# Kernel tuning notes

Hardware: AMD Instinct MI355X
Metric: run time of the kernel (lower is better)

## Reference

```python
import jax, jax.numpy as jnp
import numpy as np

DIM = 1024

def setup_inputs() -> dict:
    key = jax.random.key(0)
    k1, k2, k3, k4, k5 = jax.random.split(key, 5)
    x = jax.random.normal(k1, (8, 2048, DIM), dtype=jnp.float32)
    # nn.Linear-style params: W is [out, in], b is [out]
    s = 1.0 / np.sqrt(DIM)
    W1 = jax.random.uniform(k2, (DIM, DIM), jnp.float32, -s, s)
    b1 = jax.random.uniform(k3, (DIM,), jnp.float32, -s, s)
    W2 = jax.random.uniform(k4, (DIM, DIM), jnp.float32, -s, s)
    b2 = jax.random.uniform(k5, (DIM,), jnp.float32, -s, s)
    return {"x": x, "W1": W1, "b1": b1, "W2": W2, "b2": b2}

def reference(x, W1, b1, W2, b2):
    # NOTE: original module reuses linear_1 for BOTH V and Q (linear_3 unused)
    V = x @ W1.T + b1                      # [B,S,D]
    K = x @ W2.T + b2                      # [B,S,D]
    Q = x @ W1.T + b1                      # [B,S,D]
    scale = 1.0 / jnp.sqrt(jnp.float32(x.shape[-1]))
    scores = jnp.einsum('bkd,bqd->bkq', K, Q) * scale  # K @ Q^T, [B,S,S]
    attn = jax.nn.softmax(scores, axis=-1)
    out = jnp.einsum('bkq,bqd->bkd', attn, V)
    return out
```

## Files before the change

kernel.cpp:

```cpp
#include <hip/hip_runtime.h>
#include <hip/hip_fp16.h>
#include <cstdint>
#include <cstddef>

#define DIMK 1024
#define NBATCH 8
#define SEQ 2048

typedef _Float16 half8 __attribute__((ext_vector_type(8)));
typedef _Float16 half4_t __attribute__((ext_vector_type(4)));
typedef float float4_t __attribute__((ext_vector_type(4)));

__device__ __forceinline__ void gload16(const _Float16* g, _Float16* l) {
  __builtin_amdgcn_global_load_lds((const __attribute__((address_space(1))) void*)g,
                                   (__attribute__((address_space(3))) void*)l, 16, 0, 0);
}

#define BAR() __builtin_amdgcn_s_barrier()
#define LGKM0() asm volatile("s_waitcnt lgkmcnt(0)" ::: "memory")
#define VMW(n) asm volatile("s_waitcnt vmcnt(" #n ")" ::: "memory")
#define PRIO1() __builtin_amdgcn_s_setprio(1)
#define PRIO0() __builtin_amdgcn_s_setprio(0)

__device__ __forceinline__ void gemm256_core(
    const char* __restrict__ Ab, const char* __restrict__ Bb,
    const int ldA, const int ldB, const int NT, _Float16* lds,
    float4_t (&acc)[8][4])
{
  const int tid = threadIdx.x;
  const int lane = tid & 63, wave = tid >> 6;
  const int warp_m = wave >> 2, warp_n = wave & 3;
  const int srow = lane >> 3;
  const int scb = ((lane & 7) ^ srow) << 4;
  const int c0 = wave * 2;
  const int fr = lane & 15, fg = lane >> 4, rsw = lane & 7;

  const int xo0 = (fg ^ rsw) << 3;
  const int xo1 = ((4 + fg) ^ rsw) << 3;
  const int aro = (warp_m * 64 + fr) * 64;
  const int bro = 16384 + (warp_n * 32 + fr) * 64;

  _Float16* const sA = lds + c0 * 512;
  _Float16* const sB = lds + 16384 + c0 * 512;
  const char* const gA = Ab + (size_t)(c0 * 8 + srow) * ldA + scb;
  const char* const gB = Bb + (size_t)(c0 * 8 + srow) * ldB + scb;
  const size_t ldA8 = (size_t)ldA * 8,   ldB8 = (size_t)ldB * 8;
  const size_t ldA128 = (size_t)ldA * 128, ldB128 = (size_t)ldB * 128;

  half8 Af[4][2], Bf0[2][2], Bf1[2][2];

#define STG_A(pbuf, ob_, bot) do { \
    _Float16* _lb = sA + (pbuf) + ((bot) ? 8192 : 0); \
    const char* _g = gA + ((bot) ? ldA128 : 0) + (size_t)(ob_); \
    gload16((const _Float16*)_g, _lb); \
    gload16((const _Float16*)(_g + ldA8), _lb + 512); } while (0)
#define STG_B(pbuf, ob_, bot) do { \
    _Float16* _lb = sB + (pbuf) + ((bot) ? 8192 : 0); \
    const char* _g = gB + ((bot) ? ldB128 : 0) + (size_t)(ob_); \
    gload16((const _Float16*)_g, _lb); \
    gload16((const _Float16*)(_g + ldB8), _lb + 512); } while (0)

#define LDA2(g) do { \
    _Pragma("unroll") for (int m = 0; m < 4; ++m) { \
      Af[m][0] = *(const half8*)(pA0 + (g) * 8192 + m * 1024); \
      Af[m][1] = *(const half8*)(pA1 + (g) * 8192 + m * 1024); \
    } } while (0)
#define LDB2(g, BF) do { \
    _Pragma("unroll") for (int n = 0; n < 2; ++n) { \
      BF[n][0] = *(const half8*)(pB0 + (g) * 8192 + n * 1024); \
      BF[n][1] = *(const half8*)(pB1 + (g) * 8192 + n * 1024); \
    } } while (0)

#define QUAD(gm, gn, BF) do { \
    _Pragma("unroll") for (int m = 0; m < 4; ++m) \
    _Pragma("unroll") for (int n = 0; n < 2; ++n) \
    _Pragma("unroll") for (int kk = 0; kk < 2; ++kk) \
      acc[(gm) * 4 + m][(gn) * 2 + n] = __builtin_amdgcn_mfma_f32_16x16x32_f16( \
          Af[m][kk], BF[n][kk], acc[(gm) * 4 + m][(gn) * 2 + n], 0, 0, 0); \
  } while (0)

  STG_A(0, 0, 0); STG_B(0, 0, 0); STG_B(0, 0, 1); STG_A(0, 0, 1);
  STG_A(32768, 128, 0); STG_B(32768, 128, 0); STG_B(32768, 128, 1);
  VMW(6);
  BAR();

  int t = 0;
  for (; t + 2 < NT; ++t) {
    const int pb  = (t & 1) << 15;
    const int pbn = pb ^ 32768;
    const int o1 = (t + 1) << 7, o2 = (t + 2) << 7;
    const _Float16* pA0 = lds + pb + aro + xo0;
    const _Float16* pA1 = lds + pb + aro + xo1;
    const _Float16* pB0 = lds + pb + bro + xo0;
    const _Float16* pB1 = lds + pb + bro + xo1;
    LDA2(0); LDB2(0, Bf0);
    STG_A(pbn, o1, 1);
    BAR(); LGKM0();
    PRIO1(); QUAD(0, 0, Bf0); PRIO0();
    BAR();
    LDB2(1, Bf1);
    STG_A(pb, o2, 0);
    BAR(); LGKM0();
    PRIO1(); QUAD(0, 1, Bf1); PRIO0();
    BAR();
    LDA2(1);
    STG_B(pb, o2, 0);
    BAR(); LGKM0();
    PRIO1(); QUAD(1, 1, Bf1); PRIO0();
    BAR();
    STG_B(pb, o2, 1);
    BAR();
    PRIO1(); QUAD(1, 0, Bf0); PRIO0();
    VMW(6);
    BAR();
  }
  {
    const int pb  = (t & 1) << 15;
    const int pbn = pb ^ 32768;
    const int oL = (NT - 1) << 7;
    const _Float16* pA0 = lds + pb + aro + xo0;
    const _Float16* pA1 = lds + pb + aro + xo1;
    const _Float16* pB0 = lds + pb + bro + xo0;
    const _Float16* pB1 = lds + pb + bro + xo1;
    LDA2(0); LDB2(0, Bf0);
    STG_A(pbn, oL, 1);
    BAR(); LGKM0();
    PRIO1(); QUAD(0, 0, Bf0); PRIO0();
    BAR();
    LDB2(1, Bf1);
    BAR(); LGKM0();
    PRIO1(); QUAD(0, 1, Bf1); PRIO0();
    BAR();
    LDA2(1);
    BAR(); LGKM0();
    PRIO1(); QUAD(1, 1, Bf1); PRIO0();
    BAR();
    PRIO1(); QUAD(1, 0, Bf0); PRIO0();
    VMW(0);
    BAR();
  }
  {
    const int pb = ((NT - 1) & 1) << 15;
    const _Float16* pA0 = lds + pb + aro + xo0;
    const _Float16* pA1 = lds + pb + aro + xo1;
    const _Float16* pB0 = lds + pb + bro + xo0;
    const _Float16* pB1 = lds + pb + bro + xo1;
    LDA2(0); LDB2(0, Bf0); LDB2(1, Bf1);
    QUAD(0, 0, Bf0); QUAD(0, 1, Bf1);
    LDA2(1);
    QUAD(1, 1, Bf1); QUAD(1, 0, Bf0);
  }
#undef STG_A
#undef STG_B
#undef LDA2
#undef LDB2
#undef QUAD
}

#define ROW_LOCAL(mi) (warp_m * 64 + ((mi) & 3) * 16 + (((mi) >> 2) ? 128 : 0))
#define COL_LOCAL(nj) (warp_n * 32 + (((nj) & 1) ? 16 : 0) + (((nj) >> 1) ? 128 : 0))

__global__ __launch_bounds__(256) void prep_kernel(const float* __restrict__ x,
                                                   const float* __restrict__ W1,
                                                   const float* __restrict__ W2,
                                                   _Float16* __restrict__ xh,
                                                   _Float16* __restrict__ Wcat) {
  int i = blockIdx.x * 256 + threadIdx.x;
  if (i < 4194304) {
    float4_t v = ((const float4_t*)x)[i];
    half4_t h; h[0]=(_Float16)v[0]; h[1]=(_Float16)v[1]; h[2]=(_Float16)v[2]; h[3]=(_Float16)v[3];
    ((half4_t*)xh)[i] = h;
  } else if (i < 4456448) {
    int j = i - 4194304;
    float4_t v = ((const float4_t*)W1)[j];
    half4_t h; h[0]=(_Float16)v[0]; h[1]=(_Float16)v[1]; h[2]=(_Float16)v[2]; h[3]=(_Float16)v[3];
    ((half4_t*)Wcat)[j] = h;
  } else if (i < 4718592) {
    int j = i - 4456448;
    float4_t v = ((const float4_t*)W2)[j];
    half4_t h; h[0]=(_Float16)v[0]; h[1]=(_Float16)v[1]; h[2]=(_Float16)v[2]; h[3]=(_Float16)v[3];
    ((half4_t*)(Wcat + 1048576))[j] = h;
  }
}

__global__ __launch_bounds__(512, 2) void gemm_vk_kernel(
    const _Float16* __restrict__ xh, const _Float16* __restrict__ Wcat,
    const float* __restrict__ b1, const float* __restrict__ b2,
    _Float16* __restrict__ Vbuf, _Float16* __restrict__ Kbuf,
    _Float16* __restrict__ Vt) {
  __shared__ _Float16 lds[65536];
  const int tid = threadIdx.x, lane = tid & 63, wave = tid >> 6;
  const int warp_m = wave >> 2, warp_n = wave & 3;
  const int fr = lane & 15, rb = (lane >> 4) * 4;
  const int flat = blockIdx.x;
  const int wg = (flat & 7) * 64 + (flat >> 3);
  const int bm = wg >> 3, bn = wg & 7;
  const bool isV = bn < 4;
  const float* bias = isV ? b1 : b2;
  const int ncol0 = (bn & 3) * 256;
  float bv[4];
#pragma unroll
  for (int nj = 0; nj < 4; ++nj) bv[nj] = bias[ncol0 + COL_LOCAL(nj) + fr];

  float4_t acc[8][4] = {};
  gemm256_core((const char*)(xh + (size_t)bm * 256 * DIMK),
               (const char*)(Wcat + (size_t)bn * 256 * DIMK),
               DIMK * 2, DIMK * 2, DIMK / 64, lds, acc);

  _Float16* dst = isV ? Vbuf : Kbuf;
#pragma unroll
  for (int mi = 0; mi < 8; ++mi) {
    const int row = bm * 256 + ROW_LOCAL(mi) + rb;
#pragma unroll
    for (int nj = 0; nj < 4; ++nj) {
      const int col = ncol0 + COL_LOCAL(nj) + fr;
#pragma unroll
      for (int r = 0; r < 4; ++r)
        dst[(size_t)(row + r) * DIMK + col] = (_Float16)(acc[mi][nj][r] + bv[nj]);
    }
  }
  if (isV) {
    __syncthreads();
#pragma unroll
    for (int mi = 0; mi < 8; ++mi) {
      const int q0 = ROW_LOCAL(mi) + rb;
#pragma unroll
      for (int nj = 0; nj < 4; ++nj) {
        const int d = COL_LOCAL(nj) + fr;
        const float bb = bv[nj];
#pragma unroll
        for (int r = 0; r < 4; ++r) {
          const int q = q0 + r;
          lds[d * 256 + ((((q >> 3) ^ d) & 31) << 3) + (q & 7)] = (_Float16)(acc[mi][nj][r] + bb);
        }
      }
    }
    __syncthreads();
    const int b = bm >> 3, qb = (bm & 7) * 256;
    const size_t vtb = ((size_t)b * DIMK + ncol0) * SEQ + qb;
#pragma unroll
    for (int i = 0; i < 16; ++i) {
      const int idx = tid + i * 512;
      const int d = idx >> 5, G = idx & 31;
      half8 v = *(const half8*)(lds + d * 256 + (((G ^ d) & 31) << 3));
      *(half8*)(Vt + vtb + (size_t)d * SEQ + G * 8) = v;
    }
  }
}

__global__ __launch_bounds__(512, 2) void gemm_scores_kernel(
    const _Float16* __restrict__ Kb, const _Float16* __restrict__ Vb,
    _Float16* __restrict__ P, float* __restrict__ rsum_part) {
  __shared__ _Float16 lds[65536];
  const int tid = threadIdx.x, lane = tid & 63, wave = tid >> 6;
  const int warp_m = wave >> 2, warp_n = wave & 3;
  const int fr = lane & 15, rb = (lane >> 4) * 4;
  const int flat = blockIdx.x;
  const int wg = (flat & 7) * 64 + (flat >> 3);
  const int b = wg >> 6, loc = wg & 63, bm = loc >> 3, bn = loc & 7;

  float4_t acc[8][4] = {};
  gemm256_core((const char*)(Kb + (size_t)(b * SEQ + bm * 256) * DIMK),
               (const char*)(Vb + (size_t)(b * SEQ + bn * 256) * DIMK),
               DIMK * 2, DIMK * 2, DIMK / 64, lds, acc);

  __syncthreads();
  float* part = (float*)lds;
  _Float16* Pb = P + (size_t)b * SEQ * SEQ;
#pragma unroll
  for (int mi = 0; mi < 8; ++mi) {
    const int rl = ROW_LOCAL(mi) + rb;
#pragma unroll
    for (int r = 0; r < 4; ++r) {
      float s = 0.f;
#pragma unroll
      for (int nj = 0; nj < 4; ++nj) {
        const int col = bn * 256 + COL_LOCAL(nj) + fr;
        const _Float16 ph = (_Float16)__expf(acc[mi][nj][r] * 0.03125f);
        Pb[(size_t)(bm * 256 + rl + r) * SEQ + col] = ph;
        s += (float)ph;
      }
      s += __shfl_xor(s, 1, 64);
      s += __shfl_xor(s, 2, 64);
      s += __shfl_xor(s, 4, 64);
      s += __shfl_xor(s, 8, 64);
      if (fr == 0) part[warp_n * 256 + rl + r] = s;
    }
  }
  __syncthreads();
  if (tid < 256) {
    const float s = part[tid] + part[256 + tid] + part[512 + tid] + part[768 + tid];
    rsum_part[((size_t)b * 8 + bn) * SEQ + bm * 256 + tid] = s;
  }
}

__global__ __launch_bounds__(512, 2) void gemm_out_kernel(
    const _Float16* __restrict__ P, const _Float16* __restrict__ Vt,
    const float* __restrict__ rsum_part, float* __restrict__ out) {
  __shared__ _Float16 lds[65536];
  const int tid = threadIdx.x, lane = tid & 63, wave = tid >> 6;
  const int warp_m = wave >> 2, warp_n = wave & 3;
  const int fr = lane & 15, rb = (lane >> 4) * 4;
  const int flat = blockIdx.x;
  const int wg = (flat & 7) * 32 + (flat >> 3);
  const int b = wg >> 5, loc = wg & 31, bm = loc >> 2, bn = loc & 3;

  float4_t acc[8][4] = {};
  gemm256_core((const char*)(P + (size_t)(b * SEQ + bm * 256) * SEQ),
               (const char*)(Vt + (size_t)(b * DIMK + bn * 256) * SEQ),
               SEQ * 2, SEQ * 2, SEQ / 64, lds, acc);

  __syncthreads();
  float* invf = (float*)lds;
  if (tid < 256) {
    const float* rp = rsum_part + (size_t)b * 8 * SEQ + bm * 256 + tid;
    float s = 0.f;
#pragma unroll
    for (int j = 0; j < 8; ++j) s += rp[j * SEQ];
    invf[tid] = __builtin_amdgcn_rcpf(s);
  }
  __syncthreads();

  float* ob = out + ((size_t)b * SEQ + bm * 256) * DIMK + bn * 256;
#pragma unroll
  for (int mi = 0; mi < 8; ++mi) {
#pragma unroll
    for (int r = 0; r < 4; ++r) {
      const int row = ROW_LOCAL(mi) + rb + r;
      const float inv = invf[row];
#pragma unroll
      for (int nj = 0; nj < 4; ++nj) {
        const int col = COL_LOCAL(nj) + fr;
        ob[(size_t)row * DIMK + col] = acc[mi][nj][r] * inv;
      }
    }
  }
}

extern "C" void kernel_launch(void* const* d_in, const int* in_sizes, int n_in,
                              void* d_out, int out_size, void* d_ws, size_t ws_size,
                              hipStream_t stream) {
  const float* x  = (const float*)d_in[0];
  const float* W1 = (const float*)d_in[1];
  const float* b1 = (const float*)d_in[2];
  const float* W2 = (const float*)d_in[3];
  const float* b2 = (const float*)d_in[4];
  float* out = (float*)d_out;

  char* ws = (char*)d_ws;
  _Float16* xh   = (_Float16*)(ws);
  _Float16* Pbuf = (_Float16*)(ws);
  _Float16* Vt   = (_Float16*)(ws + 67108864);
  _Float16* Vbuf = (_Float16*)(ws + 100663296);
  _Float16* Kbuf = (_Float16*)(ws + 134217728);
  _Float16* Wcat = (_Float16*)(ws + 167772160);
  float* rsum_part = (float*)(ws + 167772160);

  prep_kernel<<<18432, 256, 0, stream>>>(x, W1, W2, xh, Wcat);
  gemm_vk_kernel<<<512, 512, 0, stream>>>(xh, Wcat, b1, b2, Vbuf, Kbuf, Vt);
  gemm_scores_kernel<<<512, 512, 0, stream>>>(Kbuf, Vbuf, Pbuf, rsum_part);
  gemm_out_kernel<<<256, 512, 0, stream>>>(Pbuf, Vt, rsum_part, out);
}
```

Baseline: 330.3 us.

## Switch GEMM core from 16x16x32 to 32x32x16 MFMA tiles

Replaces the 16x16x32 f16 MFMA fragments with 32x32x16 MFMA instructions across the shared GEMM core. This changes the LDS fragment load pattern, the accumulator layout (4x2 floatx16), and every epilogue's row and column mapping. The larger MFMA shape needs fewer LDS fragment reads per flop and fewer instructions. It also adds scheduling barriers before the MFMA blocks and drops one block barrier before the last quadrant. The new epilogue layout changes the store patterns and adds an extra shuffle step to the row-sum reduction.

```diff
diff --git a/kernel.cpp b/kernel.cpp
--- a/kernel.cpp
+++ b/kernel.cpp
@@ -10,6 +10,7 @@
 typedef _Float16 half8 __attribute__((ext_vector_type(8)));
 typedef _Float16 half4_t __attribute__((ext_vector_type(4)));
 typedef float float4_t __attribute__((ext_vector_type(4)));
+typedef float floatx16 __attribute__((ext_vector_type(16)));
 
 __device__ __forceinline__ void gload16(const _Float16* g, _Float16* l) {
   __builtin_amdgcn_global_load_lds((const __attribute__((address_space(1))) void*)g,
@@ -21,11 +22,12 @@
 #define VMW(n) asm volatile("s_waitcnt vmcnt(" #n ")" ::: "memory")
 #define PRIO1() __builtin_amdgcn_s_setprio(1)
 #define PRIO0() __builtin_amdgcn_s_setprio(0)
+#define SCHED0() __builtin_amdgcn_sched_barrier(0)
 
 __device__ __forceinline__ void gemm256_core(
     const char* __restrict__ Ab, const char* __restrict__ Bb,
     const int ldA, const int ldB, const int NT, _Float16* lds,
-    float4_t (&acc)[8][4])
+    floatx16 (&acc)[4][2])
 {
   const int tid = threadIdx.x;
   const int lane = tid & 63, wave = tid >> 6;
@@ -33,12 +35,14 @@
   const int srow = lane >> 3;
   const int scb = ((lane & 7) ^ srow) << 4;
   const int c0 = wave * 2;
-  const int fr = lane & 15, fg = lane >> 4, rsw = lane & 7;
-
-  const int xo0 = (fg ^ rsw) << 3;
-  const int xo1 = ((4 + fg) ^ rsw) << 3;
-  const int aro = (warp_m * 64 + fr) * 64;
-  const int bro = 16384 + (warp_n * 32 + fr) * 64;
+  const int m32 = lane & 31, ksel = lane >> 5, rsw = lane & 7;
+
+  const int xo0 = ((0 + ksel) ^ rsw) << 3;
+  const int xo1 = ((2 + ksel) ^ rsw) << 3;
+  const int xo2 = ((4 + ksel) ^ rsw) << 3;
+  const int xo3 = ((6 + ksel) ^ rsw) << 3;
+  const int aro = (warp_m * 64 + m32) * 64;
+  const int bro = 16384 + (warp_n * 32 + m32) * 64;
 
   _Float16* const sA = lds + c0 * 512;
   _Float16* const sB = lds + 16384 + c0 * 512;
@@ -47,7 +51,7 @@
   const size_t ldA8 = (size_t)ldA * 8,   ldB8 = (size_t)ldB * 8;
   const size_t ldA128 = (size_t)ldA * 128, ldB128 = (size_t)ldB * 128;
 
-  half8 Af[4][2], Bf0[2][2], Bf1[2][2];
+  half8 Af[2][4], Bf0[4], Bf1[4];
 
 #define STG_A(pbuf, ob_, bot) do { \
     _Float16* _lb = sA + (pbuf) + ((bot) ? 8192 : 0); \
@@ -60,23 +64,25 @@
     gload16((const _Float16*)_g, _lb); \
     gload16((const _Float16*)(_g + ldB8), _lb + 512); } while (0)
 
-#define LDA2(g) do { \
-    _Pragma("unroll") for (int m = 0; m < 4; ++m) { \
-      Af[m][0] = *(const half8*)(pA0 + (g) * 8192 + m * 1024); \
-      Af[m][1] = *(const half8*)(pA1 + (g) * 8192 + m * 1024); \
+#define LDA_G(g) do { \
+    _Pragma("unroll") for (int mt = 0; mt < 2; ++mt) { \
+      Af[mt][0] = *(const half8*)(pA0 + (g) * 8192 + mt * 2048); \
+      Af[mt][1] = *(const half8*)(pA1 + (g) * 8192 + mt * 2048); \
+      Af[mt][2] = *(const half8*)(pA2 + (g) * 8192 + mt * 2048); \
+      Af[mt][3] = *(const half8*)(pA3 + (g) * 8192 + mt * 2048); \
     } } while (0)
-#define LDB2(g, BF) do { \
-    _Pragma("unroll") for (int n = 0; n < 2; ++n) { \
-      BF[n][0] = *(const half8*)(pB0 + (g) * 8192 + n * 1024); \
-      BF[n][1] = *(const half8*)(pB1 + (g) * 8192 + n * 1024); \
-    } } while (0)
-
-#define QUAD(gm, gn, BF) do { \
-    _Pragma("unroll") for (int m = 0; m < 4; ++m) \
-    _Pragma("unroll") for (int n = 0; n < 2; ++n) \
-    _Pragma("unroll") for (int kk = 0; kk < 2; ++kk) \
-      acc[(gm) * 4 + m][(gn) * 2 + n] = __builtin_amdgcn_mfma_f32_16x16x32_f16( \
-          Af[m][kk], BF[n][kk], acc[(gm) * 4 + m][(gn) * 2 + n], 0, 0, 0); \
+#define LDB_G(g, BF) do { \
+      BF[0] = *(const half8*)(pB0 + (g) * 8192); \
+      BF[1] = *(const half8*)(pB1 + (g) * 8192); \
+      BF[2] = *(const half8*)(pB2 + (g) * 8192); \
+      BF[3] = *(const half8*)(pB3 + (g) * 8192); \
+    } while (0)
+
+#define QUAD2(mb, nt, BF) do { \
+    _Pragma("unroll") for (int mt = 0; mt < 2; ++mt) \
+    _Pragma("unroll") for (int kk = 0; kk < 4; ++kk) \
+      acc[(mb) + mt][nt] = __builtin_amdgcn_mfma_f32_32x32x16_f16( \
+          Af[mt][kk], BF[kk], acc[(mb) + mt][nt], 0, 0, 0); \
   } while (0)
 
   STG_A(0, 0, 0); STG_B(0, 0, 0); STG_B(0, 0, 1); STG_A(0, 0, 1);
@@ -91,26 +97,29 @@
     const int o1 = (t + 1) << 7, o2 = (t + 2) << 7;
     const _Float16* pA0 = lds + pb + aro + xo0;
     const _Float16* pA1 = lds + pb + aro + xo1;
+    const _Float16* pA2 = lds + pb + aro + xo2;
+    const _Float16* pA3 = lds + pb + aro + xo3;
     const _Float16* pB0 = lds + pb + bro + xo0;
     const _Float16* pB1 = lds + pb + bro + xo1;
-    LDA2(0); LDB2(0, Bf0);
+    const _Float16* pB2 = lds + pb + bro + xo2;
+    const _Float16* pB3 = lds + pb + bro + xo3;
+    LDA_G(0); LDB_G(0, Bf0);
     STG_A(pbn, o1, 1);
-    BAR(); LGKM0();
-    PRIO1(); QUAD(0, 0, Bf0); PRIO0();
-    BAR();
-    LDB2(1, Bf1);
+    BAR(); LGKM0(); SCHED0();
+    PRIO1(); QUAD2(0, 0, Bf0); PRIO0();
+    BAR();
+    LDB_G(1, Bf1);
     STG_A(pb, o2, 0);
-    BAR(); LGKM0();
-    PRIO1(); QUAD(0, 1, Bf1); PRIO0();
-    BAR();
-    LDA2(1);
+    BAR(); LGKM0(); SCHED0();
+    PRIO1(); QUAD2(0, 1, Bf1); PRIO0();
+    BAR();
+    LDA_G(1);
     STG_B(pb, o2, 0);
-    BAR(); LGKM0();
-    PRIO1(); QUAD(1, 1, Bf1); PRIO0();
+    BAR(); LGKM0(); SCHED0();
+    PRIO1(); QUAD2(2, 1, Bf1); PRIO0();
     BAR();
     STG_B(pb, o2, 1);
-    BAR();
-    PRIO1(); QUAD(1, 0, Bf0); PRIO0();
+    PRIO1(); QUAD2(2, 0, Bf0); PRIO0();
     VMW(6);
     BAR();
   }
@@ -120,22 +129,26 @@
     const int oL = (NT - 1) << 7;
     const _Float16* pA0 = lds + pb + aro + xo0;
     const _Float16* pA1 = lds + pb + aro + xo1;
+    const _Float16* pA2 = lds + pb + aro + xo2;
+    const _Float16* pA3 = lds + pb + aro + xo3;
     const _Float16* pB0 = lds + pb + bro + xo0;
     const _Float16* pB1 = lds + pb + bro + xo1;
-    LDA2(0); LDB2(0, Bf0);
+    const _Float16* pB2 = lds + pb + bro + xo2;
+    const _Float16* pB3 = lds + pb + bro + xo3;
+    LDA_G(0); LDB_G(0, Bf0);
     STG_A(pbn, oL, 1);
-    BAR(); LGKM0();
-    PRIO1(); QUAD(0, 0, Bf0); PRIO0();
-    BAR();
-    LDB2(1, Bf1);
-    BAR(); LGKM0();
-    PRIO1(); QUAD(0, 1, Bf1); PRIO0();
-    BAR();
-    LDA2(1);
-    BAR(); LGKM0();
-    PRIO1(); QUAD(1, 1, Bf1); PRIO0();
-    BAR();
-    PRIO1(); QUAD(1, 0, Bf0); PRIO0();
+    BAR(); LGKM0(); SCHED0();
+    PRIO1(); QUAD2(0, 0, Bf0); PRIO0();
+    BAR();
+    LDB_G(1, Bf1);
+    BAR(); LGKM0(); SCHED0();
+    PRIO1(); QUAD2(0, 1, Bf1); PRIO0();
+    BAR();
+    LDA_G(1);
+    BAR(); LGKM0(); SCHED0();
+    PRIO1(); QUAD2(2, 1, Bf1); PRIO0();
+    BAR();
+    PRIO1(); QUAD2(2, 0, Bf0); PRIO0();
     VMW(0);
     BAR();
   }
@@ -143,22 +156,27 @@
     const int pb = ((NT - 1) & 1) << 15;
     const _Float16* pA0 = lds + pb + aro + xo0;
     const _Float16* pA1 = lds + pb + aro + xo1;
+    const _Float16* pA2 = lds + pb + aro + xo2;
+    const _Float16* pA3 = lds + pb + aro + xo3;
     const _Float16* pB0 = lds + pb + bro + xo0;
     const _Float16* pB1 = lds + pb + bro + xo1;
-    LDA2(0); LDB2(0, Bf0); LDB2(1, Bf1);
-    QUAD(0, 0, Bf0); QUAD(0, 1, Bf1);
-    LDA2(1);
-    QUAD(1, 1, Bf1); QUAD(1, 0, Bf0);
+    const _Float16* pB2 = lds + pb + bro + xo2;
+    const _Float16* pB3 = lds + pb + bro + xo3;
+    LDA_G(0); LDB_G(0, Bf0); LDB_G(1, Bf1);
+    QUAD2(0, 0, Bf0); QUAD2(0, 1, Bf1);
+    LDA_G(1);
+    QUAD2(2, 1, Bf1); QUAD2(2, 0, Bf0);
   }
 #undef STG_A
 #undef STG_B
-#undef LDA2
-#undef LDB2
-#undef QUAD
-}
-
-#define ROW_LOCAL(mi) (warp_m * 64 + ((mi) & 3) * 16 + (((mi) >> 2) ? 128 : 0))
-#define COL_LOCAL(nj) (warp_n * 32 + (((nj) & 1) ? 16 : 0) + (((nj) >> 1) ? 128 : 0))
+#undef LDA_G
+#undef LDB_G
+#undef QUAD2
+}
+
+#define ROW32(mt) (warp_m * 64 + ((mt) & 1) * 32 + (((mt) >> 1) ? 128 : 0))
+#define COL32(nt) (warp_n * 32 + ((nt) ? 128 : 0))
+#define RL32(mt, reg) (ROW32(mt) + ((reg) & 3) + 8 * ((reg) >> 2) + 4 * ksel)
 
 __global__ __launch_bounds__(256) void prep_kernel(const float* __restrict__ x,
                                                    const float* __restrict__ W1,
@@ -191,47 +209,47 @@
   __shared__ _Float16 lds[65536];
   const int tid = threadIdx.x, lane = tid & 63, wave = tid >> 6;
   const int warp_m = wave >> 2, warp_n = wave & 3;
-  const int fr = lane & 15, rb = (lane >> 4) * 4;
+  const int m32 = lane & 31, ksel = lane >> 5;
   const int flat = blockIdx.x;
   const int wg = (flat & 7) * 64 + (flat >> 3);
   const int bm = wg >> 3, bn = wg & 7;
   const bool isV = bn < 4;
   const float* bias = isV ? b1 : b2;
   const int ncol0 = (bn & 3) * 256;
-  float bv[4];
-#pragma unroll
-  for (int nj = 0; nj < 4; ++nj) bv[nj] = bias[ncol0 + COL_LOCAL(nj) + fr];
-
-  float4_t acc[8][4] = {};
+  float bv[2];
+#pragma unroll
+  for (int nt = 0; nt < 2; ++nt) bv[nt] = bias[ncol0 + COL32(nt) + m32];
+
+  floatx16 acc[4][2] = {};
   gemm256_core((const char*)(xh + (size_t)bm * 256 * DIMK),
                (const char*)(Wcat + (size_t)bn * 256 * DIMK),
                DIMK * 2, DIMK * 2, DIMK / 64, lds, acc);
 
   _Float16* dst = isV ? Vbuf : Kbuf;
 #pragma unroll
-  for (int mi = 0; mi < 8; ++mi) {
-    const int row = bm * 256 + ROW_LOCAL(mi) + rb;
-#pragma unroll
-    for (int nj = 0; nj < 4; ++nj) {
-      const int col = ncol0 + COL_LOCAL(nj) + fr;
-#pragma unroll
-      for (int r = 0; r < 4; ++r)
-        dst[(size_t)(row + r) * DIMK + col] = (_Float16)(acc[mi][nj][r] + bv[nj]);
+  for (int mt = 0; mt < 4; ++mt) {
+#pragma unroll
+    for (int nt = 0; nt < 2; ++nt) {
+      const int col = ncol0 + COL32(nt) + m32;
+#pragma unroll
+      for (int reg = 0; reg < 16; ++reg) {
+        const int row = bm * 256 + RL32(mt, reg);
+        dst[(size_t)row * DIMK + col] = (_Float16)(acc[mt][nt][reg] + bv[nt]);
+      }
     }
   }
   if (isV) {
     __syncthreads();
 #pragma unroll
-    for (int mi = 0; mi < 8; ++mi) {
-      const int q0 = ROW_LOCAL(mi) + rb;
-#pragma unroll
-      for (int nj = 0; nj < 4; ++nj) {
-        const int d = COL_LOCAL(nj) + fr;
-        const float bb = bv[nj];
-#pragma unroll
-        for (int r = 0; r < 4; ++r) {
-          const int q = q0 + r;
-          lds[d * 256 + ((((q >> 3) ^ d) & 31) << 3) + (q & 7)] = (_Float16)(acc[mi][nj][r] + bb);
+    for (int mt = 0; mt < 4; ++mt) {
+#pragma unroll
+      for (int nt = 0; nt < 2; ++nt) {
+        const int d = COL32(nt) + m32;
+        const float bb = bv[nt];
+#pragma unroll
+        for (int reg = 0; reg < 16; ++reg) {
+          const int q = RL32(mt, reg);
+          lds[d * 256 + ((((q >> 3) ^ d) & 31) << 3) + (q & 7)] = (_Float16)(acc[mt][nt][reg] + bb);
         }
       }
     }
@@ -254,12 +272,12 @@
   __shared__ _Float16 lds[65536];
   const int tid = threadIdx.x, lane = tid & 63, wave = tid >> 6;
   const int warp_m = wave >> 2, warp_n = wave & 3;
-  const int fr = lane & 15, rb = (lane >> 4) * 4;
+  const int m32 = lane & 31, ksel = lane >> 5;
   const int flat = blockIdx.x;
   const int wg = (flat & 7) * 64 + (flat >> 3);
   const int b = wg >> 6, loc = wg & 63, bm = loc >> 3, bn = loc & 7;
 
-  float4_t acc[8][4] = {};
+  floatx16 acc[4][2] = {};
   gemm256_core((const char*)(Kb + (size_t)(b * SEQ + bm * 256) * DIMK),
                (const char*)(Vb + (size_t)(b * SEQ + bn * 256) * DIMK),
                DIMK * 2, DIMK * 2, DIMK / 64, lds, acc);
@@ -267,24 +285,24 @@
   __syncthreads();
   float* part = (float*)lds;
   _Float16* Pb = P + (size_t)b * SEQ * SEQ;
-#pragma unroll
-  for (int mi = 0; mi < 8; ++mi) {
-    const int rl = ROW_LOCAL(mi) + rb;
-#pragma unroll
-    for (int r = 0; r < 4; ++r) {
-      float s = 0.f;
-#pragma unroll
-      for (int nj = 0; nj < 4; ++nj) {
-        const int col = bn * 256 + COL_LOCAL(nj) + fr;
-        const _Float16 ph = (_Float16)__expf(acc[mi][nj][r] * 0.03125f);
-        Pb[(size_t)(bm * 256 + rl + r) * SEQ + col] = ph;
-        s += (float)ph;
-      }
+  const int colb = bn * 256 + warp_n * 32 + m32;
+#pragma unroll
+  for (int mt = 0; mt < 4; ++mt) {
+#pragma unroll
+    for (int reg = 0; reg < 16; ++reg) {
+      const int rl = RL32(mt, reg);
+      const _Float16 p0 = (_Float16)__expf(acc[mt][0][reg] * 0.03125f);
+      const _Float16 p1 = (_Float16)__expf(acc[mt][1][reg] * 0.03125f);
+      _Float16* prow = Pb + (size_t)(bm * 256 + rl) * SEQ + colb;
+      prow[0]   = p0;
+      prow[128] = p1;
+      float s = (float)p0 + (float)p1;
       s += __shfl_xor(s, 1, 64);
       s += __shfl_xor(s, 2, 64);
       s += __shfl_xor(s, 4, 64);
       s += __shfl_xor(s, 8, 64);
-      if (fr == 0) part[warp_n * 256 + rl + r] = s;
+      s += __shfl_xor(s, 16, 64);
+      if (m32 == 0) part[warp_n * 256 + rl] = s;
     }
   }
   __syncthreads();
@@ -300,12 +318,12 @@
   __shared__ _Float16 lds[65536];
   const int tid = threadIdx.x, lane = tid & 63, wave = tid >> 6;
   const int warp_m = wave >> 2, warp_n = wave & 3;
-  const int fr = lane & 15, rb = (lane >> 4) * 4;
+  const int m32 = lane & 31, ksel = lane >> 5;
   const int flat = blockIdx.x;
   const int wg = (flat & 7) * 32 + (flat >> 3);
   const int b = wg >> 5, loc = wg & 31, bm = loc >> 2, bn = loc & 3;
 
-  float4_t acc[8][4] = {};
+  floatx16 acc[4][2] = {};
   gemm256_core((const char*)(P + (size_t)(b * SEQ + bm * 256) * SEQ),
                (const char*)(Vt + (size_t)(b * DIMK + bn * 256) * SEQ),
                SEQ * 2, SEQ * 2, SEQ / 64, lds, acc);
@@ -323,15 +341,15 @@
 
   float* ob = out + ((size_t)b * SEQ + bm * 256) * DIMK + bn * 256;
 #pragma unroll
-  for (int mi = 0; mi < 8; ++mi) {
-#pragma unroll
-    for (int r = 0; r < 4; ++r) {
-      const int row = ROW_LOCAL(mi) + rb + r;
+  for (int mt = 0; mt < 4; ++mt) {
+#pragma unroll
+    for (int reg = 0; reg < 16; ++reg) {
+      const int row = RL32(mt, reg);
       const float inv = invf[row];
 #pragma unroll
-      for (int nj = 0; nj < 4; ++nj) {
-        const int col = COL_LOCAL(nj) + fr;
-        ob[(size_t)row * DIMK + col] = acc[mi][nj][r] * inv;
+      for (int nt = 0; nt < 2; ++nt) {
+        const int col = COL32(nt) + m32;
+        ob[(size_t)row * DIMK + col] = acc[mt][nt][reg] * inv;
       }
     }
   }
```

New measurement: 369.6 us. 11.9% more time.

## Software-pipeline LDS fragment reads across MFMA quadrants in GEMM core

Applied to the files above, without the earlier changes.

Splits the A fragments into separate Lo/Hi register sets and issues the LDS reads for the next quadrant, and for the next k-tile, ahead of the current MFMA block. Partial lgkmcnt waits and sched_barrier replace the full waits, and several barriers are removed from each iteration. The aim is to hide LDS read latency behind MFMA work and cut synchronisation stalls. This raises register pressure, and the hand-tuned vmcnt/lgkmcnt counts risk races if any of them is miscounted.

```diff
diff --git a/kernel.cpp b/kernel.cpp
--- a/kernel.cpp
+++ b/kernel.cpp
@@ -16,11 +16,12 @@
                                    (__attribute__((address_space(3))) void*)l, 16, 0, 0);
 }
 
-#define BAR() __builtin_amdgcn_s_barrier()
-#define LGKM0() asm volatile("s_waitcnt lgkmcnt(0)" ::: "memory")
+#define BAR() asm volatile("s_barrier" ::: "memory")
+#define LGKM(n) asm volatile("s_waitcnt lgkmcnt(" #n ")" ::: "memory")
 #define VMW(n) asm volatile("s_waitcnt vmcnt(" #n ")" ::: "memory")
 #define PRIO1() __builtin_amdgcn_s_setprio(1)
 #define PRIO0() __builtin_amdgcn_s_setprio(0)
+#define SCHED0() __builtin_amdgcn_sched_barrier(0)
 
 __device__ __forceinline__ void gemm256_core(
     const char* __restrict__ Ab, const char* __restrict__ Bb,
@@ -47,7 +48,7 @@
   const size_t ldA8 = (size_t)ldA * 8,   ldB8 = (size_t)ldB * 8;
   const size_t ldA128 = (size_t)ldA * 128, ldB128 = (size_t)ldB * 128;
 
-  half8 Af[4][2], Bf0[2][2], Bf1[2][2];
+  half8 AfLo[4][2], AfHi[4][2], Bf0[2][2], Bf1[2][2];
 
 #define STG_A(pbuf, ob_, bot) do { \
     _Float16* _lb = sA + (pbuf) + ((bot) ? 8192 : 0); \
@@ -60,100 +61,89 @@
     gload16((const _Float16*)_g, _lb); \
     gload16((const _Float16*)(_g + ldB8), _lb + 512); } while (0)
 
-#define LDA2(g) do { \
+#define RDA(DST, pbase, g) do { \
     _Pragma("unroll") for (int m = 0; m < 4; ++m) { \
-      Af[m][0] = *(const half8*)(pA0 + (g) * 8192 + m * 1024); \
-      Af[m][1] = *(const half8*)(pA1 + (g) * 8192 + m * 1024); \
+      DST[m][0] = *(const half8*)(lds + (pbase) + aro + (g) * 8192 + m * 1024 + xo0); \
+      DST[m][1] = *(const half8*)(lds + (pbase) + aro + (g) * 8192 + m * 1024 + xo1); \
     } } while (0)
-#define LDB2(g, BF) do { \
+#define RDB(DST, pbase, g) do { \
     _Pragma("unroll") for (int n = 0; n < 2; ++n) { \
-      BF[n][0] = *(const half8*)(pB0 + (g) * 8192 + n * 1024); \
-      BF[n][1] = *(const half8*)(pB1 + (g) * 8192 + n * 1024); \
+      DST[n][0] = *(const half8*)(lds + (pbase) + bro + (g) * 8192 + n * 1024 + xo0); \
+      DST[n][1] = *(const half8*)(lds + (pbase) + bro + (g) * 8192 + n * 1024 + xo1); \
     } } while (0)
 
-#define QUAD(gm, gn, BF) do { \
+#define QUAD(gm, gn, AF, BF) do { \
     _Pragma("unroll") for (int m = 0; m < 4; ++m) \
     _Pragma("unroll") for (int n = 0; n < 2; ++n) \
     _Pragma("unroll") for (int kk = 0; kk < 2; ++kk) \
       acc[(gm) * 4 + m][(gn) * 2 + n] = __builtin_amdgcn_mfma_f32_16x16x32_f16( \
-          Af[m][kk], BF[n][kk], acc[(gm) * 4 + m][(gn) * 2 + n], 0, 0, 0); \
+          AF[m][kk], BF[n][kk], acc[(gm) * 4 + m][(gn) * 2 + n], 0, 0, 0); \
   } while (0)
 
   STG_A(0, 0, 0); STG_B(0, 0, 0); STG_B(0, 0, 1); STG_A(0, 0, 1);
   STG_A(32768, 128, 0); STG_B(32768, 128, 0); STG_B(32768, 128, 1);
-  VMW(6);
+  VMW(8);
   BAR();
+  RDA(AfLo, 0, 0);
+  RDB(Bf0, 0, 0);
 
   int t = 0;
   for (; t + 2 < NT; ++t) {
-    const int pb  = (t & 1) << 15;
-    const int pbn = pb ^ 32768;
+    const int pb = (t & 1) << 15, pbn = pb ^ 32768;
     const int o1 = (t + 1) << 7, o2 = (t + 2) << 7;
-    const _Float16* pA0 = lds + pb + aro + xo0;
-    const _Float16* pA1 = lds + pb + aro + xo1;
-    const _Float16* pB0 = lds + pb + bro + xo0;
-    const _Float16* pB1 = lds + pb + bro + xo1;
-    LDA2(0); LDB2(0, Bf0);
+    VMW(6);
+    RDB(Bf1, pb, 1);
+    LGKM(4); SCHED0();
+    PRIO1(); QUAD(0, 0, AfLo, Bf0); PRIO0();
     STG_A(pbn, o1, 1);
-    BAR(); LGKM0();
-    PRIO1(); QUAD(0, 0, Bf0); PRIO0();
-    BAR();
-    LDB2(1, Bf1);
+    BAR();
+    RDA(AfHi, pb, 1);
+    LGKM(8); SCHED0();
+    PRIO1(); QUAD(0, 1, AfLo, Bf1); PRIO0();
     STG_A(pb, o2, 0);
-    BAR(); LGKM0();
-    PRIO1(); QUAD(0, 1, Bf1); PRIO0();
-    BAR();
-    LDA2(1);
+    BAR();
+    VMW(6);
+    LGKM(0); SCHED0();
+    PRIO1(); QUAD(1, 1, AfHi, Bf1); PRIO0();
     STG_B(pb, o2, 0);
-    BAR(); LGKM0();
-    PRIO1(); QUAD(1, 1, Bf1); PRIO0();
-    BAR();
+    BAR();
+    PRIO1(); QUAD(1, 0, AfHi, Bf0); PRIO0();
+    RDA(AfLo, pbn, 0);
+    RDB(Bf0, pbn, 0);
+    VMW(6);
     STG_B(pb, o2, 1);
     BAR();
-    PRIO1(); QUAD(1, 0, Bf0); PRIO0();
+  }
+  {
+    const int pb = (t & 1) << 15, pbn = pb ^ 32768;
+    const int oL = (NT - 1) << 7;
     VMW(6);
-    BAR();
-  }
-  {
-    const int pb  = (t & 1) << 15;
-    const int pbn = pb ^ 32768;
-    const int oL = (NT - 1) << 7;
-    const _Float16* pA0 = lds + pb + aro + xo0;
-    const _Float16* pA1 = lds + pb + aro + xo1;
-    const _Float16* pB0 = lds + pb + bro + xo0;
-    const _Float16* pB1 = lds + pb + bro + xo1;
-    LDA2(0); LDB2(0, Bf0);
+    RDB(Bf1, pb, 1);
+    LGKM(4); SCHED0();
+    PRIO1(); QUAD(0, 0, AfLo, Bf0); PRIO0();
     STG_A(pbn, oL, 1);
-    BAR(); LGKM0();
-    PRIO1(); QUAD(0, 0, Bf0); PRIO0();
-    BAR();
-    LDB2(1, Bf1);
-    BAR(); LGKM0();
-    PRIO1(); QUAD(0, 1, Bf1); PRIO0();
-    BAR();
-    LDA2(1);
-    BAR(); LGKM0();
-    PRIO1(); QUAD(1, 1, Bf1); PRIO0();
-    BAR();
-    PRIO1(); QUAD(1, 0, Bf0); PRIO0();
+    BAR();
+    RDA(AfHi, pb, 1);
+    LGKM(8); SCHED0();
+    PRIO1(); QUAD(0, 1, AfLo, Bf1); PRIO0();
+    BAR();
+    LGKM(0); SCHED0();
+    PRIO1(); QUAD(1, 1, AfHi, Bf1); PRIO0();
+    PRIO1(); QUAD(1, 0, AfHi, Bf0); PRIO0();
     VMW(0);
     BAR();
   }
   {
     const int pb = ((NT - 1) & 1) << 15;
-    const _Float16* pA0 = lds + pb + aro + xo0;
-    const _Float16* pA1 = lds + pb + aro + xo1;
-    const _Float16* pB0 = lds + pb + bro + xo0;
-    const _Float16* pB1 = lds + pb + bro + xo1;
-    LDA2(0); LDB2(0, Bf0); LDB2(1, Bf1);
-    QUAD(0, 0, Bf0); QUAD(0, 1, Bf1);
-    LDA2(1);
-    QUAD(1, 1, Bf1); QUAD(1, 0, Bf0);
+    RDA(AfLo, pb, 0); RDB(Bf0, pb, 0); RDB(Bf1, pb, 1);
+    QUAD(0, 0, AfLo, Bf0); QUAD(0, 1, AfLo, Bf1);
+    RDA(AfHi, pb, 1);
+    QUAD(1, 1, AfHi, Bf1); QUAD(1, 0, AfHi, Bf0);
   }
 #undef STG_A
 #undef STG_B
-#undef LDA2
-#undef LDB2
+#undef RDA
+#undef RDB
 #undef QUAD
 }
 
```

New measurement: 327.1 us. No clear change (-1.0%).
